# Optimization experiments

Hardware: AMD Instinct MI355X
Metric: run time of the kernel (lower is better)

Reference implementation:

```python
import jax, jax.numpy as jnp
import numpy as np

B, T, NC, NK, H, W = 2, 4, 3, 16, 180, 320
K = 3
PAD = 1
SCALE = 4
K2 = K * K
CIN_D = T * NK  # deformable conv input channels = group_of_frames * num_kernels


def conv2d(x, w, b=None, pad=PAD):
    y = jax.lax.conv_general_dilated(
        x, w, (1, 1), [(pad, pad), (pad, pad)],
        dimension_numbers=('NCHW', 'OIHW', 'NCHW'))
    if b is not None:
        y = y + b[None, :, None, None]
    return y


def convlstm(X, w, b, W_ci, W_cf, W_co):
    # X: (B, T, NC, H, W) -> (B, T, NK, H, W); peephole ConvLSTM
    Bn = X.shape[0]
    h0 = jnp.zeros((Bn, NK, H, W), X.dtype)
    c0 = jnp.zeros_like(h0)

    def step(carry, xt):
        h, c = carry
        g = conv2d(jnp.concatenate([xt, h], axis=1), w, b)  # (B, 4*NK, H, W)
        ig, fg, cg, og = jnp.split(g, 4, axis=1)
        i = jax.nn.sigmoid(ig + W_ci * c)
        f = jax.nn.sigmoid(fg + W_cf * c)
        c = f * c + i * jnp.tanh(cg)
        o = jax.nn.sigmoid(og + W_co * c)
        h = o * jnp.tanh(c)
        return (h, c), h

    _, hs = jax.lax.scan(step, (h0, c0), jnp.swapaxes(X, 0, 1))
    return jnp.swapaxes(hs, 0, 1)  # (B, T, NK, H, W)


def deform_conv(x, off_w, off_b, mod_w, mod_b, w, b):
    # Modulated deformable conv v2 (torchvision deform_conv2d semantics)
    Bn, Cin, Hi, Wi = x.shape
    off = conv2d(x, off_w, off_b).reshape(Bn, K2, 2, Hi, Wi)  # (dy, dx) per tap
    mask = 2.0 * jax.nn.sigmoid(conv2d(x, mod_w, mod_b))       # (B, K2, H, W)
    dy, dx = off[:, :, 0], off[:, :, 1]
    ky, kx = jnp.meshgrid(jnp.arange(K), jnp.arange(K), indexing='ij')
    base_y = jnp.arange(Hi, dtype=x.dtype)[None, None, :, None] - PAD + ky.reshape(1, K2, 1, 1).astype(x.dtype)
    base_x = jnp.arange(Wi, dtype=x.dtype)[None, None, None, :] - PAD + kx.reshape(1, K2, 1, 1).astype(x.dtype)
    py = base_y + dy  # (B, K2, H, W) float sampling positions
    px = base_x + dx
    y0 = jnp.floor(py)
    x0 = jnp.floor(px)

    def gather(yi, xi):
        valid = ((yi >= 0) & (yi < Hi) & (xi >= 0) & (xi < Wi)).astype(x.dtype)
        yc = jnp.clip(yi, 0, Hi - 1).astype(jnp.int32)
        xc = jnp.clip(xi, 0, Wi - 1).astype(jnp.int32)
        v = jax.vmap(lambda xb, yb, xib: xb[:, yb, xib])(x, yc, xc)  # (B, C, K2, H, W)
        return v * valid[:, None]

    wy1 = py - y0
    wx1 = px - x0
    samp = (((1 - wy1) * (1 - wx1))[:, None] * gather(y0, x0)
            + ((1 - wy1) * wx1)[:, None] * gather(y0, x0 + 1)
            + (wy1 * (1 - wx1))[:, None] * gather(y0 + 1, x0)
            + (wy1 * wx1)[:, None] * gather(y0 + 1, x0 + 1))
    samp = samp * mask[:, None]  # (B, Cin, K2, H, W)
    out = jnp.einsum('bckhw,ock->bohw', samp, w.reshape(w.shape[0], Cin, K2))
    return out + b[None, :, None, None]


def pixel_shuffle(x, r):
    Bn, Crr, Hi, Wi = x.shape
    C = Crr // (r * r)
    x = x.reshape(Bn, C, r, r, Hi, Wi).transpose(0, 1, 4, 2, 5, 3)
    return x.reshape(Bn, C, Hi * r, Wi * r)


def setup_inputs() -> dict:
    key = jax.random.key(0)
    ks = jax.random.split(key, 16)
    s = lambda k, shape, sc=0.05: jax.random.normal(k, shape, jnp.float32) * sc
    return {
        'X': jax.random.uniform(ks[0], (B, T, NC, H, W), jnp.float32),
        'lstm_w': s(ks[1], (4 * NK, NC + NK, K, K)),
        'lstm_b': s(ks[2], (4 * NK,)),
        'W_ci': s(ks[3], (NK, H, W)),
        'W_cf': s(ks[4], (NK, H, W)),
        'W_co': s(ks[5], (NK, H, W)),
        'off_w': s(ks[6], (2 * K2, CIN_D, K, K), 0.01),
        'off_b': jnp.zeros((2 * K2,), jnp.float32),
        'mod_w': s(ks[7], (K2, CIN_D, K, K), 0.01),
        'mod_b': jnp.zeros((K2,), jnp.float32),
        'def_w': s(ks[8], (NK, CIN_D, K, K)),
        'def_b': s(ks[9], (NK,)),
        'out_w': s(ks[10], (NC * SCALE ** 2, NK, K, K)),
        'out_b': s(ks[11], (NC * SCALE ** 2,)),
    }


def reference(X, lstm_w, lstm_b, W_ci, W_cf, W_co, off_w, off_b, mod_w, mod_b, def_w, def_b, out_w, out_b):
    hs = convlstm(X, lstm_w, lstm_b, W_ci, W_cf, W_co)   # (B, T, NK, H, W)
    x = hs.reshape(hs.shape[0], T * NK, H, W)            # chunk(dim=1)+squeeze+cat(dim=1)
    x = deform_conv(x, off_w, off_b, mod_w, mod_b, def_w, def_b)  # (B, NK, H, W)
    x = conv2d(x, out_w, out_b)                          # (B, NC*scale^2, H, W)
    return jnp.clip(pixel_shuffle(x, SCALE), 0.0, 255.0)
```

## Files before the change

### kernel.cpp

```cpp
#include <hip/hip_runtime.h>
#include <hip/hip_bf16.h>

#define Bn 2
#define Tn 4
#define NCc 3
#define NKc 16
#define Hc 180
#define Wc 320
#define HWc (Hc * Wc)
#define NPIX (Bn * HWc)
#define CIN_LSTM 19
#define GATES 64
#define CIN_D 64
#define TAPS_L (CIN_LSTM * 9)
#define TAPS_D (CIN_D * 9)
#define TAPS_O (NKc * 9)

typedef __hip_bfloat16 bf16;
typedef float f32x4 __attribute__((ext_vector_type(4)));
typedef float f32x2 __attribute__((ext_vector_type(2)));

__device__ __forceinline__ float getv(const float* p, long i) { return p[i]; }
__device__ __forceinline__ float getv(const bf16* p, long i) {
    unsigned int u = ((unsigned int)((const unsigned short*)p)[i]) << 16;
    return __uint_as_float(u);
}
__device__ __forceinline__ void putv(float* p, long i, float v) { p[i] = v; }
__device__ __forceinline__ void putv(bf16* p, long i, float v) { p[i] = __float2bfloat16(v); }
__device__ __forceinline__ float sigm(float x) { return 1.0f / (1.0f + __expf(-x)); }
__device__ __forceinline__ float tanh_(float x) { return 1.0f - 2.0f / (__expf(2.0f * x) + 1.0f); }

__device__ __forceinline__ void load4(const float* row, int x0, float* d) {
    const float4 v = *(const float4*)(row + x0);
    d[0] = v.x; d[1] = v.y; d[2] = v.z; d[3] = v.w;
}
__device__ __forceinline__ void load4(const bf16* row, int x0, float* d) {
    ushort4 u = *(const ushort4*)((const unsigned short*)row + x0);
    d[0] = __uint_as_float(((unsigned int)u.x) << 16);
    d[1] = __uint_as_float(((unsigned int)u.y) << 16);
    d[2] = __uint_as_float(((unsigned int)u.z) << 16);
    d[3] = __uint_as_float(((unsigned int)u.w) << 16);
}

__device__ __forceinline__ int xcd_chunked(int i, int nwg) {
    int q = nwg >> 3, r = nwg & 7;
    int xcd = i & 7, idx = i >> 3;
    return (xcd < r ? xcd * (q + 1) : r * (q + 1) + (xcd - r) * q) + idx;
}

__device__ __forceinline__ void om_wait()
{
    asm volatile("s_waitcnt vmcnt(0)" ::: "memory");
    __builtin_amdgcn_sched_barrier(0);
}

__device__ __forceinline__ void om_issue12(
    const float* p0, const float* p1, const float* p2,
    f32x4& a0, f32x4& b0, float& h00, float& h01,
    f32x4& a1, f32x4& b1, float& h10, float& h11,
    f32x4& a2, f32x4& b2, float& h20, float& h21)
{
    asm volatile(
        "global_load_dwordx4 %[A0], %[p0], off\n\t"
        "global_load_dwordx4 %[B0], %[p0], off offset:16\n\t"
        "global_load_dword   %[H00], %[p0], off offset:-4\n\t"
        "global_load_dword   %[H01], %[p0], off offset:32\n\t"
        "global_load_dwordx4 %[A1], %[p1], off\n\t"
        "global_load_dwordx4 %[B1], %[p1], off offset:16\n\t"
        "global_load_dword   %[H10], %[p1], off offset:-4\n\t"
        "global_load_dword   %[H11], %[p1], off offset:32\n\t"
        "global_load_dwordx4 %[A2], %[p2], off\n\t"
        "global_load_dwordx4 %[B2], %[p2], off offset:16\n\t"
        "global_load_dword   %[H20], %[p2], off offset:-4\n\t"
        "global_load_dword   %[H21], %[p2], off offset:32\n\t"
        : [A0]"=&v"(a0), [B0]"=&v"(b0), [H00]"=&v"(h00), [H01]"=&v"(h01),
          [A1]"=&v"(a1), [B1]"=&v"(b1), [H10]"=&v"(h10), [H11]"=&v"(h11),
          [A2]"=&v"(a2), [B2]"=&v"(b2), [H20]"=&v"(h20), [H21]"=&v"(h21)
        : [p0]"v"(p0), [p1]"v"(p1), [p2]"v"(p2));
}

__device__ __forceinline__ void lstm_issue12(
    const float* p0, const float* p1, const float* p2, const float* p3,
    f32x4& a0, float& l0, float& r0,
    f32x4& a1, float& l1, float& r1,
    f32x4& a2, float& l2, float& r2,
    f32x4& a3, float& l3, float& r3)
{
    asm volatile(
        "global_load_dwordx4 %[A0], %[P0], off\n\t"
        "global_load_dword   %[L0], %[P0], off offset:-4\n\t"
        "global_load_dword   %[R0], %[P0], off offset:16\n\t"
        "global_load_dwordx4 %[A1], %[P1], off\n\t"
        "global_load_dword   %[L1], %[P1], off offset:-4\n\t"
        "global_load_dword   %[R1], %[P1], off offset:16\n\t"
        "global_load_dwordx4 %[A2], %[P2], off\n\t"
        "global_load_dword   %[L2], %[P2], off offset:-4\n\t"
        "global_load_dword   %[R2], %[P2], off offset:16\n\t"
        "global_load_dwordx4 %[A3], %[P3], off\n\t"
        "global_load_dword   %[L3], %[P3], off offset:-4\n\t"
        "global_load_dword   %[R3], %[P3], off offset:16\n\t"
        : [A0]"=&v"(a0), [L0]"=&v"(l0), [R0]"=&v"(r0),
          [A1]"=&v"(a1), [L1]"=&v"(l1), [R1]"=&v"(r1),
          [A2]"=&v"(a2), [L2]"=&v"(l2), [R2]"=&v"(r2),
          [A3]"=&v"(a3), [L3]"=&v"(l3), [R3]"=&v"(r3)
        : [P0]"v"(p0), [P1]"v"(p1), [P2]"v"(p2), [P3]"v"(p3));
}

__device__ __forceinline__ void dfm_issue9w(
    const float* base, const int (&o)[9], f32x2 (&v)[9])
{
    asm volatile(
        "global_load_dwordx2 %[V0], %[O0], %[B]\n\t"
        "global_load_dwordx2 %[V1], %[O1], %[B]\n\t"
        "global_load_dwordx2 %[V2], %[O2], %[B]\n\t"
        "global_load_dwordx2 %[V3], %[O3], %[B]\n\t"
        "global_load_dwordx2 %[V4], %[O4], %[B]\n\t"
        "global_load_dwordx2 %[V5], %[O5], %[B]\n\t"
        "global_load_dwordx2 %[V6], %[O6], %[B]\n\t"
        "global_load_dwordx2 %[V7], %[O7], %[B]\n\t"
        "global_load_dwordx2 %[V8], %[O8], %[B]\n\t"
        : [V0]"=&v"(v[0]), [V1]"=&v"(v[1]), [V2]"=&v"(v[2]),
          [V3]"=&v"(v[3]), [V4]"=&v"(v[4]), [V5]"=&v"(v[5]),
          [V6]"=&v"(v[6]), [V7]"=&v"(v[7]), [V8]"=&v"(v[8])
        : [B]"s"(base),
          [O0]"v"(o[0]), [O1]"v"(o[1]), [O2]"v"(o[2]),
          [O3]"v"(o[3]), [O4]"v"(o[4]), [O5]"v"(o[5]),
          [O6]"v"(o[6]), [O7]"v"(o[7]), [O8]"v"(o[8]));
}

__global__ void __launch_bounds__(256) k_detect(const void* lstm_w_raw, int* flag)
{
    __shared__ int bad;
    if (threadIdx.x == 0) bad = 0;
    __syncthreads();
    const unsigned short* u = (const unsigned short*)lstm_w_raw;
    int local = 0;
    for (int i = threadIdx.x; i < GATES * TAPS_L; i += 256) {
        unsigned int f32 = ((unsigned int)u[i]) << 16;
        float v = __uint_as_float(f32);
        if (!(fabsf(v) <= 64.0f)) local = 1;
    }
    if (local) atomicOr(&bad, 1);
    __syncthreads();
    if (threadIdx.x == 0) flag[0] = bad ? 0 : 1;
}

template <typename S>
__device__ __forceinline__ void conv_plane2r(
    const S* __restrict__ src, int cin, int y0, int x0, int kc,
    const float* __restrict__ sw, float (&acc)[2][4][4])
{
    float xs[4][6];
#pragma unroll
    for (int r = 0; r < 4; r++) {
        int yy = y0 - 1 + r;
        if (yy >= 0 && yy < Hc) {
            const S* row = src + (long)yy * Wc;
            xs[r][0] = (x0 > 0) ? getv(row, x0 - 1) : 0.0f;
            load4(row, x0, &xs[r][1]);
            xs[r][5] = (x0 + 4 < Wc) ? getv(row, x0 + 4) : 0.0f;
        } else {
#pragma unroll
            for (int j = 0; j < 6; j++) xs[r][j] = 0.0f;
        }
    }
    float4 wq[9];
#pragma unroll
    for (int t9 = 0; t9 < 9; t9++)
        wq[t9] = *(const float4*)&sw[(((cin * 9 + t9) * 16) + kc) * 4];
#pragma unroll
    for (int ky = 0; ky < 3; ky++) {
#pragma unroll
        for (int kx = 0; kx < 3; kx++) {
            const float4 w = wq[ky * 3 + kx];
#pragma unroll
            for (int px = 0; px < 4; px++) {
                float v0 = xs[ky][px + kx];
                float v1 = xs[ky + 1][px + kx];
                acc[0][0][px] += w.x * v0;  acc[1][0][px] += w.x * v1;
                acc[0][1][px] += w.y * v0;  acc[1][1][px] += w.y * v1;
                acc[0][2][px] += w.z * v0;  acc[1][2][px] += w.z * v1;
                acc[0][3][px] += w.w * v0;  acc[1][3][px] += w.w * v1;
            }
        }
    }
}

template <typename T>
__device__ __forceinline__ void lstm2r_body(
    const T* __restrict__ X, const T* __restrict__ lstm_w, const T* __restrict__ lstm_b,
    const T* __restrict__ Wci, const T* __restrict__ Wcf, const T* __restrict__ Wco,
    float* __restrict__ c_buf, float* __restrict__ xcat, int t,
    float* sw, float* sb)
{
    for (int i = threadIdx.x; i < GATES * TAPS_L; i += 256) {
        int co = i / TAPS_L, tap = i - co * TAPS_L;
        int kc = co & 15, g = co >> 4;
        sw[(tap * 16 + kc) * 4 + g] = getv(lstm_w, i);
    }
    if (threadIdx.x < GATES) sb[threadIdx.x] = getv(lstm_b, threadIdx.x);
    __syncthreads();

    int blk = xcd_chunked(blockIdx.x, Bn * 90 * 5);
    int seg = blk % 5; int rem = blk / 5;
    int yp = rem % 90; int b = rem / 90;
    int y0 = yp * 2;
    int kc = threadIdx.x >> 4, pl = threadIdx.x & 15;
    int x0 = seg * 64 + pl * 4;

    float acc[2][4][4];
#pragma unroll
    for (int px = 0; px < 4; px++) {
#pragma unroll
        for (int r = 0; r < 2; r++) {
            acc[r][0][px] = sb[kc];
            acc[r][1][px] = sb[16 + kc];
            acc[r][2][px] = sb[32 + kc];
            acc[r][3][px] = sb[48 + kc];
        }
    }

    const T* xt = X + (long)(b * Tn + t) * NCc * HWc;
#pragma unroll 1
    for (int cin = 0; cin < NCc; cin++)
        conv_plane2r(xt + (long)cin * HWc, cin, y0, x0, kc, sw, acc);

    if (t > 0) {
        const float* hp = xcat + ((long)b * CIN_D + (t - 1) * NKc) * HWc;
        long ro[4]; float vm[4];
#pragma unroll
        for (int r = 0; r < 4; r++) {
            int yy = y0 - 1 + r;
            vm[r] = (yy >= 0 && yy < Hc) ? 1.0f : 0.0f;
            ro[r] = (long)min(max(yy, 0), Hc - 1) * Wc + x0;
        }
        const float m0 = (x0 > 0) ? 1.0f : 0.0f;
        const float m1 = (x0 + 4 < Wc) ? 1.0f : 0.0f;

#pragma unroll 1
        for (int cin = 0; cin < NKc; cin++) {
            const float* xc = hp + (long)cin * HWc;
            f32x4 a0, a1, a2, a3;
            float l0, l1, l2, l3, rh0, rh1, rh2, rh3;
            lstm_issue12(xc + ro[0], xc + ro[1], xc + ro[2], xc + ro[3],
                         a0, l0, rh0, a1, l1, rh1, a2, l2, rh2, a3, l3, rh3);
            float4 wq[9];
#pragma unroll
            for (int t9 = 0; t9 < 9; t9++)
                wq[t9] = *(const float4*)&sw[((((cin + NCc) * 9 + t9) * 16) + kc) * 4];
            om_wait();
            float xs[4][6];
#pragma unroll
            for (int r = 0; r < 4; r++) {
                const f32x4 a = (r == 0) ? a0 : (r == 1) ? a1 : (r == 2) ? a2 : a3;
                const float ll = (r == 0) ? l0 : (r == 1) ? l1 : (r == 2) ? l2 : l3;
                const float rr = (r == 0) ? rh0 : (r == 1) ? rh1 : (r == 2) ? rh2 : rh3;
                xs[r][0] = ll * vm[r] * m0;
                xs[r][1] = a.x * vm[r]; xs[r][2] = a.y * vm[r];
                xs[r][3] = a.z * vm[r]; xs[r][4] = a.w * vm[r];
                xs[r][5] = rr * vm[r] * m1;
            }
#pragma unroll
            for (int ky = 0; ky < 3; ky++) {
#pragma unroll
                for (int kx = 0; kx < 3; kx++) {
                    const float4 w = wq[ky * 3 + kx];
#pragma unroll
                    for (int px = 0; px < 4; px++) {
                        float v0 = xs[ky][px + kx];
                        float v1 = xs[ky + 1][px + kx];
                        acc[0][0][px] += w.x * v0;  acc[1][0][px] += w.x * v1;
                        acc[0][1][px] += w.y * v0;  acc[1][1][px] += w.y * v1;
                        acc[0][2][px] += w.z * v0;  acc[1][2][px] += w.z * v1;
                        acc[0][3][px] += w.w * v0;  acc[1][3][px] += w.w * v1;
                    }
                }
            }
        }
    }

#pragma unroll
    for (int r = 0; r < 2; r++) {
        int y = y0 + r;
        long pbase = (long)y * Wc + x0;
        float* cb = c_buf + (long)(b * NKc + kc) * HWc + pbase;
        float cprev[4];
        if (t > 0) {
            const float4 cv = *(const float4*)cb;
            cprev[0] = cv.x; cprev[1] = cv.y; cprev[2] = cv.z; cprev[3] = cv.w;
        } else {
            cprev[0] = cprev[1] = cprev[2] = cprev[3] = 0.0f;
        }
        float wci[4], wcf[4], wco[4];
        load4(Wci + (long)kc * HWc + pbase, 0, wci);
        load4(Wcf + (long)kc * HWc + pbase, 0, wcf);
        load4(Wco + (long)kc * HWc + pbase, 0, wco);

        float cn4[4], h4[4];
#pragma unroll
        for (int px = 0; px < 4; px++) {
            float ii = sigm(acc[r][0][px] + wci[px] * cprev[px]);
            float ff = sigm(acc[r][1][px] + wcf[px] * cprev[px]);
            float cn = ff * cprev[px] + ii * tanh_(acc[r][2][px]);
            float oo = sigm(acc[r][3][px] + wco[px] * cn);
            cn4[px] = cn; h4[px] = oo * tanh_(cn);
        }
        *(float4*)cb = make_float4(cn4[0], cn4[1], cn4[2], cn4[3]);
        *(float4*)(xcat + ((long)b * CIN_D + t * NKc + kc) * HWc + pbase) =
            make_float4(h4[0], h4[1], h4[2], h4[3]);
    }
}

__global__ void __launch_bounds__(256) k_lstm2(
    const void* X, const void* lstm_w, const void* lstm_b,
    const void* Wci, const void* Wcf, const void* Wco,
    const int* __restrict__ flag,
    float* c_buf, float* xcat, int t)
{
    __shared__ float sw[TAPS_L * GATES];
    __shared__ float sb[GATES];
    if (flag[0])
        lstm2r_body<bf16>((const bf16*)X, (const bf16*)lstm_w, (const bf16*)lstm_b,
                          (const bf16*)Wci, (const bf16*)Wcf, (const bf16*)Wco,
                          c_buf, xcat, t, sw, sb);
    else
        lstm2r_body<float>((const float*)X, (const float*)lstm_w, (const float*)lstm_b,
                           (const float*)Wci, (const float*)Wcf, (const float*)Wco,
                           c_buf, xcat, t, sw, sb);
}

template <typename T>
__device__ __forceinline__ void offmod12_body(
    const float* __restrict__ xcat,
    const T* __restrict__ off_w, const T* __restrict__ off_b,
    const T* __restrict__ mod_w, const T* __restrict__ mod_b,
    float* __restrict__ offbuf, float* __restrict__ maskbuf,
    float* sw, float* sb)
{
    int rb = xcd_chunked(blockIdx.x, 450);
    int type = rb & 1;
    int chunk = rb >> 1;
    const int nslot = type ? 12 : 16;

    for (int i = threadIdx.x; i < TAPS_D * nslot; i += 256) {
        int tap = i / nslot, j = i - tap * nslot;
        int o = type ? 16 + j : j;
        float v = 0.0f;
        if (o < 18) v = getv(off_w, (long)o * TAPS_D + tap);
        else if (o < 27) v = getv(mod_w, (long)(o - 18) * TAPS_D + tap);
        sw[tap * nslot + j] = v;
    }
    if (threadIdx.x < nslot) {
        int o = (type ? 16 : 0) + threadIdx.x;
        sb[threadIdx.x] = (o < 18) ? getv(off_b, o)
                        : (o < 27 ? getv(mod_b, o - 18) : 0.0f);
    }
    __syncthreads();

    int og = threadIdx.x >> 6, lane = threadIdx.x & 63;
    long p0 = (long)chunk * 512 + lane * 8;
    int b = (int)(p0 / HWc);
    int p = (int)(p0 - (long)b * HWc);
    int y = p / Wc, x0 = p - (p / Wc) * Wc;

    const int per = type ? 3 : 4;
    int jbase = og * per;

    const float* xb = xcat + (long)b * CIN_D * HWc;
    long yo[3]; float vm[3];
#pragma unroll
    for (int ky = 0; ky < 3; ky++) {
        int yy = y + ky - 1;
        vm[ky] = (yy >= 0 && yy < Hc) ? 1.0f : 0.0f;
        yo[ky] = (long)min(max(yy, 0), Hc - 1) * Wc + x0;
    }
    const float m0 = (x0 > 0) ? 1.0f : 0.0f;
    const float m1 = (x0 + 8 < Wc) ? 1.0f : 0.0f;

    float acc[4][8];
#pragma unroll
    for (int j = 0; j < 4; j++) {
        float bv = (j < per) ? sb[jbase + j] : 0.0f;
#pragma unroll
        for (int px = 0; px < 8; px++) acc[j][px] = bv;
    }

    if (type == 0) {
#pragma unroll 1
        for (int cin = 0; cin < CIN_D; cin++) {
            const float* xc = xb + (long)cin * HWc;
            f32x4 a0, b0v, a1, b1v, a2, b2v;
            float h00, h01, h10, h11, h20, h21;
            om_issue12(xc + yo[0], xc + yo[1], xc + yo[2],
                       a0, b0v, h00, h01, a1, b1v, h10, h11, a2, b2v, h20, h21);
            float4 wr[9];
#pragma unroll
            for (int t9 = 0; t9 < 9; t9++)
                wr[t9] = *(const float4*)&sw[(cin * 9 + t9) * 16 + jbase];
            om_wait();
            float xs[3][10];
#pragma unroll
            for (int ky = 0; ky < 3; ky++) {
                const f32x4 a = (ky == 0) ? a0 : (ky == 1) ? a1 : a2;
                const f32x4 bb = (ky == 0) ? b0v : (ky == 1) ? b1v : b2v;
                const float hh0 = (ky == 0) ? h00 : (ky == 1) ? h10 : h20;
                const float hh1 = (ky == 0) ? h01 : (ky == 1) ? h11 : h21;
                xs[ky][0] = hh0 * vm[ky] * m0;
                xs[ky][1] = a.x * vm[ky]; xs[ky][2] = a.y * vm[ky];
                xs[ky][3] = a.z * vm[ky]; xs[ky][4] = a.w * vm[ky];
                xs[ky][5] = bb.x * vm[ky]; xs[ky][6] = bb.y * vm[ky];
                xs[ky][7] = bb.z * vm[ky]; xs[ky][8] = bb.w * vm[ky];
                xs[ky][9] = hh1 * vm[ky] * m1;
            }
#pragma unroll
            for (int ky = 0; ky < 3; ky++) {
#pragma unroll
                for (int kx = 0; kx < 3; kx++) {
                    const float4 wq = wr[ky * 3 + kx];
#pragma unroll
                    for (int px = 0; px < 8; px++) {
                        float v = xs[ky][px + kx];
                        acc[0][px] += wq.x * v;
                        acc[1][px] += wq.y * v;
                        acc[2][px] += wq.z * v;
                        acc[3][px] += wq.w * v;
                    }
                }
            }
        }
    } else {
#pragma unroll 1
        for (int cin = 0; cin < CIN_D; cin++) {
            const float* xc = xb + (long)cin * HWc;
            f32x4 a0, b0v, a1, b1v, a2, b2v;
            float h00, h01, h10, h11, h20, h21;
            om_issue12(xc + yo[0], xc + yo[1], xc + yo[2],
                       a0, b0v, h00, h01, a1, b1v, h10, h11, a2, b2v, h20, h21);
            float3 wr[9];
#pragma unroll
            for (int t9 = 0; t9 < 9; t9++) {
                const float* wp = &sw[(cin * 9 + t9) * 12 + jbase];
                wr[t9] = make_float3(wp[0], wp[1], wp[2]);
            }
            om_wait();
            float xs[3][10];
#pragma unroll
            for (int ky = 0; ky < 3; ky++) {
                const f32x4 a = (ky == 0) ? a0 : (ky == 1) ? a1 : a2;
                const f32x4 bb = (ky == 0) ? b0v : (ky == 1) ? b1v : b2v;
                const float hh0 = (ky == 0) ? h00 : (ky == 1) ? h10 : h20;
                const float hh1 = (ky == 0) ? h01 : (ky == 1) ? h11 : h21;
                xs[ky][0] = hh0 * vm[ky] * m0;
                xs[ky][1] = a.x * vm[ky]; xs[ky][2] = a.y * vm[ky];
                xs[ky][3] = a.z * vm[ky]; xs[ky][4] = a.w * vm[ky];
                xs[ky][5] = bb.x * vm[ky]; xs[ky][6] = bb.y * vm[ky];
                xs[ky][7] = bb.z * vm[ky]; xs[ky][8] = bb.w * vm[ky];
                xs[ky][9] = hh1 * vm[ky] * m1;
            }
#pragma unroll
            for (int ky = 0; ky < 3; ky++) {
#pragma unroll
                for (int kx = 0; kx < 3; kx++) {
                    const float3 wq = wr[ky * 3 + kx];
#pragma unroll
                    for (int px = 0; px < 8; px++) {
                        float v = xs[ky][px + kx];
                        acc[0][px] += wq.x * v;
                        acc[1][px] += wq.y * v;
                        acc[2][px] += wq.z * v;
                    }
                }
            }
        }
    }

    long pbase = (long)y * Wc + x0;
#pragma unroll
    for (int j = 0; j < 4; j++) {
        if (j >= per) break;
        int o = (type ? 16 : 0) + jbase + j;
        if (o >= 27) break;
        if (o < 18) {
            float* dst = offbuf + ((long)b * 18 + o) * HWc + pbase;
            *(float4*)dst = make_float4(acc[j][0], acc[j][1], acc[j][2], acc[j][3]);
            *(float4*)(dst + 4) = make_float4(acc[j][4], acc[j][5], acc[j][6], acc[j][7]);
        } else {
            float* dst = maskbuf + ((long)b * 9 + (o - 18)) * HWc + pbase;
            *(float4*)dst = make_float4(2.0f * sigm(acc[j][0]), 2.0f * sigm(acc[j][1]),
                                        2.0f * sigm(acc[j][2]), 2.0f * sigm(acc[j][3]));
            *(float4*)(dst + 4) = make_float4(2.0f * sigm(acc[j][4]), 2.0f * sigm(acc[j][5]),
                                              2.0f * sigm(acc[j][6]), 2.0f * sigm(acc[j][7]));
        }
    }
}

__global__ void __launch_bounds__(256) k_offmod(
    const float* xcat, const void* off_w, const void* off_b,
    const void* mod_w, const void* mod_b, const int* __restrict__ flag,
    float* offbuf, float* maskbuf)
{
    __shared__ float sw[TAPS_D * 16];
    __shared__ float sb[16];
    if (flag[0])
        offmod12_body<bf16>(xcat, (const bf16*)off_w, (const bf16*)off_b,
                            (const bf16*)mod_w, (const bf16*)mod_b, offbuf, maskbuf, sw, sb);
    else
        offmod12_body<float>(xcat, (const float*)off_w, (const float*)off_b,
                             (const float*)mod_w, (const float*)mod_b, offbuf, maskbuf, sw, sb);
}

template <typename T>
__device__ __forceinline__ void deform5_body(
    const float* __restrict__ xcat, const float* __restrict__ offbuf,
    const float* __restrict__ maskbuf,
    const T* __restrict__ def_w, const T* __restrict__ def_b,
    float* __restrict__ dcout, float* sw, float* sb)
{
    for (int i = threadIdx.x; i < NKc * TAPS_D; i += 256) {
        int co = i / TAPS_D;
        int tap = i - co * TAPS_D;
        sw[tap * NKc + co] = getv(def_w, i);
    }
    if (threadIdx.x < NKc) sb[threadIdx.x] = getv(def_b, threadIdx.x);
    __syncthreads();

    int blk = xcd_chunked(blockIdx.x, NPIX / 256);
    int idx0 = blk * 256;
    int b = idx0 / HWc;
    int p = idx0 - b * HWc + threadIdx.x;
    int y = p / Wc, x = p - (p / Wc) * Wc;

    float w00[9], w01[9], w10[9], w11[9];
    int o0[9], o1[9];
    float sel[9];
#pragma unroll
    for (int k = 0; k < 9; k++) {
        int ky = k / 3, kx = k - (k / 3) * 3;
        float dy = offbuf[((long)b * 18 + 2 * k) * HWc + p];
        float dx = offbuf[((long)b * 18 + 2 * k + 1) * HWc + p];
        float m = maskbuf[((long)b * 9 + k) * HWc + p];
        float py = (float)(y - 1 + ky) + dy;
        float px = (float)(x - 1 + kx) + dx;
        float y0f = floorf(py), x0f = floorf(px);
        int y0 = (int)y0f, x0 = (int)x0f;
        float wy1 = py - y0f, wx1 = px - x0f;
        float a00 = (1.0f - wy1) * (1.0f - wx1) * m;
        float a01 = (1.0f - wy1) * wx1 * m;
        float a10 = wy1 * (1.0f - wx1) * m;
        float a11 = wy1 * wx1 * m;
        bool vy0 = (y0 >= 0) && (y0 < Hc);
        bool vy1 = (y0 + 1 >= 0) && (y0 + 1 < Hc);
        bool vx0 = (x0 >= 0) && (x0 < Wc);
        bool vx1 = (x0 + 1 >= 0) && (x0 + 1 < Wc);
        w00[k] = (vy0 && vx0) ? a00 : 0.0f;
        w01[k] = (vy0 && vx1) ? a01 : 0.0f;
        w10[k] = (vy1 && vx0) ? a10 : 0.0f;
        w11[k] = (vy1 && vx1) ? a11 : 0.0f;
        int yc0 = min(max(y0, 0), Hc - 1);
        int yc1 = min(max(y0 + 1, 0), Hc - 1);
        int xc0 = min(max(x0, 0), Wc - 1);
        int xc1 = min(max(x0 + 1, 0), Wc - 1);
        o0[k] = (yc0 * Wc + xc0) * 4;
        o1[k] = (yc1 * Wc + xc0) * 4;
        sel[k] = (xc1 > xc0) ? 1.0f : 0.0f;
    }

    float acc[NKc];
#pragma unroll
    for (int i = 0; i < NKc; i++) acc[i] = sb[i];

    const float* xb = xcat + (long)b * CIN_D * HWc;
#pragma unroll 1
    for (int cin = 0; cin < CIN_D; cin++) {
        const float* xc = xb + (long)cin * HWc;
        f32x2 u0[9], u1[9];
        dfm_issue9w(xc, o0, u0);
        dfm_issue9w(xc, o1, u1);
        om_wait();
        float s[9];
#pragma unroll
        for (int k = 0; k < 9; k++) {
            float v01 = u0[k].x + sel[k] * (u0[k].y - u0[k].x);
            float v11 = u1[k].x + sel[k] * (u1[k].y - u1[k].x);
            s[k] = w00[k] * u0[k].x + w01[k] * v01 +
                   w10[k] * u1[k].x + w11[k] * v11;
        }
#pragma unroll
        for (int k = 0; k < 9; k++) {
            const float* wrow = &sw[(cin * 9 + k) * NKc];
#pragma unroll
            for (int co = 0; co < NKc; co++) acc[co] += wrow[co] * s[k];
        }
    }

#pragma unroll
    for (int co = 0; co < NKc; co++)
        dcout[((long)b * NKc + co) * HWc + p] = acc[co];
}

__global__ void __launch_bounds__(256) k_deform(
    const float* xcat, const float* offbuf, const float* maskbuf,
    const void* def_w, const void* def_b, const int* __restrict__ flag,
    float* dcout)
{
    __shared__ float sw[TAPS_D * NKc];
    __shared__ float sb[NKc];
    if (flag[0])
        deform5_body<bf16>(xcat, offbuf, maskbuf, (const bf16*)def_w, (const bf16*)def_b,
                           dcout, sw, sb);
    else
        deform5_body<float>(xcat, offbuf, maskbuf, (const float*)def_w, (const float*)def_b,
                            dcout, sw, sb);
}

template <typename T>
__device__ __forceinline__ void outconv6_body(
    const float* __restrict__ dcout, const T* __restrict__ out_w,
    const T* __restrict__ out_b, T* __restrict__ out, float* sw, float* sb)
{
    int rb = xcd_chunked(blockIdx.x, 900);
    int type = rb & 1;
    int chunk = rb >> 1;

    for (int i = threadIdx.x; i < 24 * TAPS_O; i += 256) {
        int o = i / TAPS_O, tap = i - o * TAPS_O;
        int slot = (o / 6) * 8 + (o % 6);
        sw[tap * 32 + slot] = getv(out_w, (long)(type * 24 + o) * TAPS_O + tap);
    }
    if (threadIdx.x < 24) sb[threadIdx.x] = getv(out_b, type * 24 + threadIdx.x);
    __syncthreads();

    int og = threadIdx.x >> 6, lane = threadIdx.x & 63;
    long p0 = ((long)chunk * 64 + lane) * 4;
    int b = (int)(p0 / HWc);
    int p = (int)(p0 - (long)b * HWc);
    int y = p / Wc, x0 = p - (p / Wc) * Wc;

    float acc[6][4];
#pragma unroll
    for (int j = 0; j < 6; j++) {
        float bv = sb[og * 6 + j];
#pragma unroll
        for (int px = 0; px < 4; px++) acc[j][px] = bv;
    }

    const float* xb = dcout + (long)b * NKc * HWc;
#pragma unroll 1
    for (int cin = 0; cin < NKc; cin++) {
        const float* xc = xb + (long)cin * HWc;
        float xs[3][6];
#pragma unroll
        for (int ky = 0; ky < 3; ky++) {
            int yy = y + ky - 1;
            if (yy >= 0 && yy < Hc) {
                const float* row = xc + (long)yy * Wc;
                xs[ky][0] = (x0 > 0) ? row[x0 - 1] : 0.0f;
                load4(row, x0, &xs[ky][1]);
                xs[ky][5] = (x0 + 4 < Wc) ? row[x0 + 4] : 0.0f;
            } else {
#pragma unroll
                for (int j = 0; j < 6; j++) xs[ky][j] = 0.0f;
            }
        }
        float4 wa[9]; float2 wb[9];
#pragma unroll
        for (int t9 = 0; t9 < 9; t9++) {
            const float* wp = &sw[(cin * 9 + t9) * 32 + og * 8];
            wa[t9] = *(const float4*)wp;
            wb[t9] = *(const float2*)(wp + 4);
        }
#pragma unroll
        for (int ky = 0; ky < 3; ky++) {
#pragma unroll
            for (int kx = 0; kx < 3; kx++) {
                const float4 w0 = wa[ky * 3 + kx];
                const float2 w1 = wb[ky * 3 + kx];
#pragma unroll
                for (int px = 0; px < 4; px++) {
                    float v = xs[ky][px + kx];
                    acc[0][px] += w0.x * v;  acc[1][px] += w0.y * v;
                    acc[2][px] += w0.z * v;  acc[3][px] += w0.w * v;
                    acc[4][px] += w1.x * v;  acc[5][px] += w1.y * v;
                }
            }
        }
    }

#pragma unroll
    for (int j = 0; j < 6; j++) {
        int co = type * 24 + og * 6 + j;
        int cc = co >> 4;
        int r = co & 15;
        int ii = r >> 2, jj = r & 3;
        long ob = (((long)b * 3 + cc) * (Hc * 4) + (y * 4 + ii)) * (long)(Wc * 4);
#pragma unroll
        for (int px = 0; px < 4; px++) {
            float v = fminf(fmaxf(acc[j][px], 0.0f), 255.0f);
            putv(out, ob + (x0 + px) * 4 + jj, v);
        }
    }
}

__global__ void __launch_bounds__(256) k_outconv(
    const float* dcout, const void* out_w, const void* out_b,
    const int* __restrict__ flag, void* out)
{
    __shared__ float sw[TAPS_O * 32];
    __shared__ float sb[24];
    if (flag[0])
        outconv6_body<bf16>(dcout, (const bf16*)out_w, (const bf16*)out_b, (bf16*)out, sw, sb);
    else
        outconv6_body<float>(dcout, (const float*)out_w, (const float*)out_b, (float*)out, sw, sb);
}

extern "C" void kernel_launch(void* const* d_in, const int* in_sizes, int n_in,
                              void* d_out, int out_size, void* d_ws, size_t ws_size,
                              hipStream_t stream) {
    const void* X      = d_in[0];
    const void* lstm_w = d_in[1];
    const void* lstm_b = d_in[2];
    const void* Wci    = d_in[3];
    const void* Wcf    = d_in[4];
    const void* Wco    = d_in[5];
    const void* off_w  = d_in[6];
    const void* off_b  = d_in[7];
    const void* mod_w  = d_in[8];
    const void* mod_b  = d_in[9];
    const void* def_w  = d_in[10];
    const void* def_b  = d_in[11];
    const void* out_w  = d_in[12];
    const void* out_b  = d_in[13];

    int* flag = (int*)d_ws;
    float* W = (float*)d_ws + 64;
    size_t o = 0;
    float* c_buf   = W + o; o += (size_t)Bn * NKc * HWc;
    float* xcat    = W + o; o += (size_t)Bn * CIN_D * HWc;
    float* offbuf  = W + o; o += (size_t)Bn * 18 * HWc;
    float* maskbuf = W + o; o += (size_t)Bn * 9 * HWc;
    float* dcout   = W + o; o += (size_t)Bn * NKc * HWc;

    dim3 blk(256);
    dim3 gridP(NPIX / 256);
    dim3 gridL2(Bn * (Hc / 2) * 5);
    dim3 gridOM(2 * (NPIX / 512));
    dim3 gridC2(2 * (NPIX / 4 / 64));

    k_detect<<<1, blk, 0, stream>>>(lstm_w, flag);
    for (int t = 0; t < Tn; t++) {
        k_lstm2<<<gridL2, blk, 0, stream>>>(X, lstm_w, lstm_b, Wci, Wcf, Wco,
                                            flag, c_buf, xcat, t);
    }
    k_offmod<<<gridOM, blk, 0, stream>>>(xcat, off_w, off_b, mod_w, mod_b, flag,
                                         offbuf, maskbuf);
    k_deform<<<gridP, blk, 0, stream>>>(xcat, offbuf, maskbuf, def_w, def_b, flag, dcout);
    k_outconv<<<gridC2, blk, 0, stream>>>(dcout, out_w, out_b, flag, d_out);
}
```

Baseline: 592.1 us.

## Use coalesced 4-pixel lane groups with shuffle-based halos in offset/mask conv

Each lane in the offset/mask conv now loads two 4-pixel groups that are 256 pixels apart, instead of 8 contiguous pixels. A wave's dwordx4 loads therefore cover contiguous 1 KB spans. Left and right halo values come from neighbouring lanes through cross-lane shuffles, and only the block's edge pixels get separate scalar loads. The aim is better load coalescing and fewer redundant halo loads, at the cost of added shuffle instructions and more setup. The type-0 and type-1 loops are also merged into one loop with a branch inside it.

```diff
diff --git a/kernel.cpp b/kernel.cpp
--- a/kernel.cpp
+++ b/kernel.cpp
@@ -54,29 +54,35 @@
     __builtin_amdgcn_sched_barrier(0);
 }
 
-__device__ __forceinline__ void om_issue12(
-    const float* p0, const float* p1, const float* p2,
-    f32x4& a0, f32x4& b0, float& h00, float& h01,
-    f32x4& a1, f32x4& b1, float& h10, float& h11,
-    f32x4& a2, f32x4& b2, float& h20, float& h21)
+__device__ __forceinline__ void om13_issue(
+    const float* a0p, const float* a1p, const float* a2p,
+    const float* b0p, const float* b1p, const float* b2p,
+    const float* l0p, const float* l1p, const float* l2p,
+    const float* r0p, const float* r1p, const float* r2p,
+    f32x4& A0, f32x4& A1, f32x4& A2, f32x4& B0, f32x4& B1, f32x4& B2,
+    float& l0, float& l1, float& l2, float& r0, float& r1, float& r2)
 {
     asm volatile(
-        "global_load_dwordx4 %[A0], %[p0], off\n\t"
-        "global_load_dwordx4 %[B0], %[p0], off offset:16\n\t"
-        "global_load_dword   %[H00], %[p0], off offset:-4\n\t"
-        "global_load_dword   %[H01], %[p0], off offset:32\n\t"
-        "global_load_dwordx4 %[A1], %[p1], off\n\t"
-        "global_load_dwordx4 %[B1], %[p1], off offset:16\n\t"
-        "global_load_dword   %[H10], %[p1], off offset:-4\n\t"
-        "global_load_dword   %[H11], %[p1], off offset:32\n\t"
-        "global_load_dwordx4 %[A2], %[p2], off\n\t"
-        "global_load_dwordx4 %[B2], %[p2], off offset:16\n\t"
-        "global_load_dword   %[H20], %[p2], off offset:-4\n\t"
-        "global_load_dword   %[H21], %[p2], off offset:32\n\t"
-        : [A0]"=&v"(a0), [B0]"=&v"(b0), [H00]"=&v"(h00), [H01]"=&v"(h01),
-          [A1]"=&v"(a1), [B1]"=&v"(b1), [H10]"=&v"(h10), [H11]"=&v"(h11),
-          [A2]"=&v"(a2), [B2]"=&v"(b2), [H20]"=&v"(h20), [H21]"=&v"(h21)
-        : [p0]"v"(p0), [p1]"v"(p1), [p2]"v"(p2));
+        "global_load_dwordx4 %[A0], %[a0], off\n\t"
+        "global_load_dwordx4 %[A1], %[a1], off\n\t"
+        "global_load_dwordx4 %[A2], %[a2], off\n\t"
+        "global_load_dwordx4 %[B0], %[b0], off\n\t"
+        "global_load_dwordx4 %[B1], %[b1], off\n\t"
+        "global_load_dwordx4 %[B2], %[b2], off\n\t"
+        "global_load_dword %[L0], %[l0p], off\n\t"
+        "global_load_dword %[L1], %[l1p], off\n\t"
+        "global_load_dword %[L2], %[l2p], off\n\t"
+        "global_load_dword %[R0], %[r0p], off\n\t"
+        "global_load_dword %[R1], %[r1p], off\n\t"
+        "global_load_dword %[R2], %[r2p], off\n\t"
+        : [A0]"=&v"(A0), [A1]"=&v"(A1), [A2]"=&v"(A2),
+          [B0]"=&v"(B0), [B1]"=&v"(B1), [B2]"=&v"(B2),
+          [L0]"=&v"(l0), [L1]"=&v"(l1), [L2]"=&v"(l2),
+          [R0]"=&v"(r0), [R1]"=&v"(r1), [R2]"=&v"(r2)
+        : [a0]"v"(a0p), [a1]"v"(a1p), [a2]"v"(a2p),
+          [b0]"v"(b0p), [b1]"v"(b1p), [b2]"v"(b2p),
+          [l0p]"v"(l0p), [l1p]"v"(l1p), [l2p]"v"(l2p),
+          [r0p]"v"(r0p), [r1p]"v"(r1p), [r2p]"v"(r2p));
 }
 
 __device__ __forceinline__ void lstm_issue12(
@@ -330,7 +336,7 @@
 }
 
 template <typename T>
-__device__ __forceinline__ void offmod12_body(
+__device__ __forceinline__ void offmod13_body(
     const float* __restrict__ xcat,
     const T* __restrict__ off_w, const T* __restrict__ off_b,
     const T* __restrict__ mod_w, const T* __restrict__ mod_b,
@@ -358,138 +364,173 @@
     __syncthreads();
 
     int og = threadIdx.x >> 6, lane = threadIdx.x & 63;
-    long p0 = (long)chunk * 512 + lane * 8;
-    int b = (int)(p0 / HWc);
-    int p = (int)(p0 - (long)b * HWc);
-    int y = p / Wc, x0 = p - (p / Wc) * Wc;
+
+    long pg[2]; pg[0] = (long)chunk * 512 + 4 * lane; pg[1] = pg[0] + 256;
+    int bg[2], ppg[2];
+    int yo[2][3]; float vm[2][3], mL[2], mR[2];
+    const float* xbg[2];
+#pragma unroll
+    for (int g = 0; g < 2; g++) {
+        int b = (int)(pg[g] / HWc);
+        int pp = (int)(pg[g] - (long)b * HWc);
+        int y = pp / Wc, x = pp - (pp / Wc) * Wc;
+        bg[g] = b; ppg[g] = pp;
+        xbg[g] = xcat + (long)b * CIN_D * HWc;
+#pragma unroll
+        for (int ky = 0; ky < 3; ky++) {
+            int yy = y + ky - 1;
+            vm[g][ky] = (yy >= 0 && yy < Hc) ? 1.0f : 0.0f;
+            yo[g][ky] = min(max(yy, 0), Hc - 1) * Wc + x;
+        }
+        mL[g] = (x > 0) ? 1.0f : 0.0f;
+        mR[g] = (x + 4 < Wc) ? 1.0f : 0.0f;
+    }
+    const float *eLp[3], *eRp[3];
+    {
+        long pL = (long)chunk * 512;
+        int b = (int)(pL / HWc); int pp = (int)(pL - (long)b * HWc);
+        int y = pp / Wc, x = pp - (pp / Wc) * Wc;
+#pragma unroll
+        for (int ky = 0; ky < 3; ky++)
+            eLp[ky] = xcat + (long)b * CIN_D * HWc
+                    + (long)min(max(y + ky - 1, 0), Hc - 1) * Wc + x - 1;
+        long pR = (long)chunk * 512 + 511;
+        b = (int)(pR / HWc); pp = (int)(pR - (long)b * HWc);
+        y = pp / Wc; x = pp - (pp / Wc) * Wc;
+#pragma unroll
+        for (int ky = 0; ky < 3; ky++)
+            eRp[ky] = xcat + (long)b * CIN_D * HWc
+                    + (long)min(max(y + ky - 1, 0), Hc - 1) * Wc + x + 1;
+    }
 
     const int per = type ? 3 : 4;
     int jbase = og * per;
-
-    const float* xb = xcat + (long)b * CIN_D * HWc;
-    long yo[3]; float vm[3];
-#pragma unroll
-    for (int ky = 0; ky < 3; ky++) {
-        int yy = y + ky - 1;
-        vm[ky] = (yy >= 0 && yy < Hc) ? 1.0f : 0.0f;
-        yo[ky] = (long)min(max(yy, 0), Hc - 1) * Wc + x0;
-    }
-    const float m0 = (x0 > 0) ? 1.0f : 0.0f;
-    const float m1 = (x0 + 8 < Wc) ? 1.0f : 0.0f;
-
-    float acc[4][8];
+    const int upl = (lane + 63) & 63, dnl = (lane + 1) & 63;
+
+    float acc[4][2][4];
 #pragma unroll
     for (int j = 0; j < 4; j++) {
         float bv = (j < per) ? sb[jbase + j] : 0.0f;
 #pragma unroll
-        for (int px = 0; px < 8; px++) acc[j][px] = bv;
-    }
-
-    if (type == 0) {
+        for (int g = 0; g < 2; g++)
+#pragma unroll
+            for (int px = 0; px < 4; px++) acc[j][g][px] = bv;
+    }
+
 #pragma unroll 1
-        for (int cin = 0; cin < CIN_D; cin++) {
-            const float* xc = xb + (long)cin * HWc;
-            f32x4 a0, b0v, a1, b1v, a2, b2v;
-            float h00, h01, h10, h11, h20, h21;
-            om_issue12(xc + yo[0], xc + yo[1], xc + yo[2],
-                       a0, b0v, h00, h01, a1, b1v, h10, h11, a2, b2v, h20, h21);
-            float4 wr[9];
+    for (int cin = 0; cin < CIN_D; cin++) {
+        const long coff = (long)cin * HWc;
+        const float* c0 = xbg[0] + coff;
+        const float* c1 = xbg[1] + coff;
+        f32x4 A[3], B[3]; float el[3], er[3];
+        om13_issue(c0 + yo[0][0], c0 + yo[0][1], c0 + yo[0][2],
+                   c1 + yo[1][0], c1 + yo[1][1], c1 + yo[1][2],
+                   eLp[0] + coff, eLp[1] + coff, eLp[2] + coff,
+                   eRp[0] + coff, eRp[1] + coff, eRp[2] + coff,
+                   A[0], A[1], A[2], B[0], B[1], B[2],
+                   el[0], el[1], el[2], er[0], er[1], er[2]);
+        float4 wr4[9]; float3 wr3[9];
+        if (type == 0) {
 #pragma unroll
             for (int t9 = 0; t9 < 9; t9++)
-                wr[t9] = *(const float4*)&sw[(cin * 9 + t9) * 16 + jbase];
-            om_wait();
-            float xs[3][10];
+                wr4[t9] = *(const float4*)&sw[(cin * 9 + t9) * 16 + jbase];
+        } else {
+#pragma unroll
+            for (int t9 = 0; t9 < 9; t9++) {
+                const float* wp = &sw[(cin * 9 + t9) * 12 + jbase];
+                wr3[t9] = make_float3(wp[0], wp[1], wp[2]);
+            }
+        }
+        om_wait();
+
+        float xs0[3][6], xs1[3][6];
+#pragma unroll
+        for (int ky = 0; ky < 3; ky++) {
+            float aw = A[ky].w, ax = A[ky].x, bw = B[ky].w, bx = B[ky].x;
+            float sAw = __shfl(aw, upl);
+            float sAx = __shfl(ax, dnl);
+            float sBw = __shfl(bw, upl);
+            float sBx = __shfl(bx, dnl);
+            float B0x = __shfl(bx, 0);
+            float A63w = __shfl(aw, 63);
+            float g0l = (lane == 0) ? el[ky] : sAw;
+            float g0r = (lane == 63) ? B0x : sAx;
+            float g1l = (lane == 0) ? A63w : sBw;
+            float g1r = (lane == 63) ? er[ky] : sBx;
+            float v0 = vm[0][ky], v1 = vm[1][ky];
+            xs0[ky][0] = g0l * v0 * mL[0];
+            xs0[ky][1] = A[ky].x * v0; xs0[ky][2] = A[ky].y * v0;
+            xs0[ky][3] = A[ky].z * v0; xs0[ky][4] = A[ky].w * v0;
+            xs0[ky][5] = g0r * v0 * mR[0];
+            xs1[ky][0] = g1l * v1 * mL[1];
+            xs1[ky][1] = B[ky].x * v1; xs1[ky][2] = B[ky].y * v1;
+            xs1[ky][3] = B[ky].z * v1; xs1[ky][4] = B[ky].w * v1;
+            xs1[ky][5] = g1r * v1 * mR[1];
+        }
+
+        if (type == 0) {
 #pragma unroll
             for (int ky = 0; ky < 3; ky++) {
-                const f32x4 a = (ky == 0) ? a0 : (ky == 1) ? a1 : a2;
-                const f32x4 bb = (ky == 0) ? b0v : (ky == 1) ? b1v : b2v;
-                const float hh0 = (ky == 0) ? h00 : (ky == 1) ? h10 : h20;
-                const float hh1 = (ky == 0) ? h01 : (ky == 1) ? h11 : h21;
-                xs[ky][0] = hh0 * vm[ky] * m0;
-                xs[ky][1] = a.x * vm[ky]; xs[ky][2] = a.y * vm[ky];
-                xs[ky][3] = a.z * vm[ky]; xs[ky][4] = a.w * vm[ky];
-                xs[ky][5] = bb.x * vm[ky]; xs[ky][6] = bb.y * vm[ky];
-                xs[ky][7] = bb.z * vm[ky]; xs[ky][8] = bb.w * vm[ky];
-                xs[ky][9] = hh1 * vm[ky] * m1;
-            }
-#pragma unroll
-            for (int ky = 0; ky < 3; ky++) {
 #pragma unroll
                 for (int kx = 0; kx < 3; kx++) {
-                    const float4 wq = wr[ky * 3 + kx];
-#pragma unroll
-                    for (int px = 0; px < 8; px++) {
-                        float v = xs[ky][px + kx];
-                        acc[0][px] += wq.x * v;
-                        acc[1][px] += wq.y * v;
-                        acc[2][px] += wq.z * v;
-                        acc[3][px] += wq.w * v;
+                    const float4 wq = wr4[ky * 3 + kx];
+#pragma unroll
+                    for (int px = 0; px < 4; px++) {
+                        float u = xs0[ky][px + kx];
+                        acc[0][0][px] += wq.x * u;
+                        acc[1][0][px] += wq.y * u;
+                        acc[2][0][px] += wq.z * u;
+                        acc[3][0][px] += wq.w * u;
+                        float w2 = xs1[ky][px + kx];
+                        acc[0][1][px] += wq.x * w2;
+                        acc[1][1][px] += wq.y * w2;
+                        acc[2][1][px] += wq.z * w2;
+                        acc[3][1][px] += wq.w * w2;
                     }
                 }
             }
-        }
-    } else {
-#pragma unroll 1
-        for (int cin = 0; cin < CIN_D; cin++) {
-            const float* xc = xb + (long)cin * HWc;
-            f32x4 a0, b0v, a1, b1v, a2, b2v;
-            float h00, h01, h10, h11, h20, h21;
-            om_issue12(xc + yo[0], xc + yo[1], xc + yo[2],
-                       a0, b0v, h00, h01, a1, b1v, h10, h11, a2, b2v, h20, h21);
-            float3 wr[9];
-#pragma unroll
-            for (int t9 = 0; t9 < 9; t9++) {
-                const float* wp = &sw[(cin * 9 + t9) * 12 + jbase];
-                wr[t9] = make_float3(wp[0], wp[1], wp[2]);
-            }
-            om_wait();
-            float xs[3][10];
+        } else {
 #pragma unroll
             for (int ky = 0; ky < 3; ky++) {
-                const f32x4 a = (ky == 0) ? a0 : (ky == 1) ? a1 : a2;
-                const f32x4 bb = (ky == 0) ? b0v : (ky == 1) ? b1v : b2v;
-                const float hh0 = (ky == 0) ? h00 : (ky == 1) ? h10 : h20;
-                const float hh1 = (ky == 0) ? h01 : (ky == 1) ? h11 : h21;
-                xs[ky][0] = hh0 * vm[ky] * m0;
-                xs[ky][1] = a.x * vm[ky]; xs[ky][2] = a.y * vm[ky];
-                xs[ky][3] = a.z * vm[ky]; xs[ky][4] = a.w * vm[ky];
-                xs[ky][5] = bb.x * vm[ky]; xs[ky][6] = bb.y * vm[ky];
-                xs[ky][7] = bb.z * vm[ky]; xs[ky][8] = bb.w * vm[ky];
-                xs[ky][9] = hh1 * vm[ky] * m1;
-            }
-#pragma unroll
-            for (int ky = 0; ky < 3; ky++) {
 #pragma unroll
                 for (int kx = 0; kx < 3; kx++) {
-                    const float3 wq = wr[ky * 3 + kx];
-#pragma unroll
-                    for (int px = 0; px < 8; px++) {
-                        float v = xs[ky][px + kx];
-                        acc[0][px] += wq.x * v;
-                        acc[1][px] += wq.y * v;
-                        acc[2][px] += wq.z * v;
+                    const float3 wq = wr3[ky * 3 + kx];
+#pragma unroll
+                    for (int px = 0; px < 4; px++) {
+                        float u = xs0[ky][px + kx];
+                        acc[0][0][px] += wq.x * u;
+                        acc[1][0][px] += wq.y * u;
+                        acc[2][0][px] += wq.z * u;
+                        float w2 = xs1[ky][px + kx];
+                        acc[0][1][px] += wq.x * w2;
+                        acc[1][1][px] += wq.y * w2;
+                        acc[2][1][px] += wq.z * w2;
                     }
                 }
             }
         }
     }
 
-    long pbase = (long)y * Wc + x0;
 #pragma unroll
     for (int j = 0; j < 4; j++) {
         if (j >= per) break;
         int o = (type ? 16 : 0) + jbase + j;
         if (o >= 27) break;
         if (o < 18) {
-            float* dst = offbuf + ((long)b * 18 + o) * HWc + pbase;
-            *(float4*)dst = make_float4(acc[j][0], acc[j][1], acc[j][2], acc[j][3]);
-            *(float4*)(dst + 4) = make_float4(acc[j][4], acc[j][5], acc[j][6], acc[j][7]);
+#pragma unroll
+            for (int g = 0; g < 2; g++) {
+                float* dst = offbuf + ((long)bg[g] * 18 + o) * HWc + ppg[g];
+                *(float4*)dst = make_float4(acc[j][g][0], acc[j][g][1],
+                                            acc[j][g][2], acc[j][g][3]);
+            }
         } else {
-            float* dst = maskbuf + ((long)b * 9 + (o - 18)) * HWc + pbase;
-            *(float4*)dst = make_float4(2.0f * sigm(acc[j][0]), 2.0f * sigm(acc[j][1]),
-                                        2.0f * sigm(acc[j][2]), 2.0f * sigm(acc[j][3]));
-            *(float4*)(dst + 4) = make_float4(2.0f * sigm(acc[j][4]), 2.0f * sigm(acc[j][5]),
-                                              2.0f * sigm(acc[j][6]), 2.0f * sigm(acc[j][7]));
+#pragma unroll
+            for (int g = 0; g < 2; g++) {
+                float* dst = maskbuf + ((long)bg[g] * 9 + (o - 18)) * HWc + ppg[g];
+                *(float4*)dst = make_float4(
+                    2.0f * sigm(acc[j][g][0]), 2.0f * sigm(acc[j][g][1]),
+                    2.0f * sigm(acc[j][g][2]), 2.0f * sigm(acc[j][g][3]));
+            }
         }
     }
 }
@@ -502,10 +543,10 @@
     __shared__ float sw[TAPS_D * 16];
     __shared__ float sb[16];
     if (flag[0])
-        offmod12_body<bf16>(xcat, (const bf16*)off_w, (const bf16*)off_b,
+        offmod13_body<bf16>(xcat, (const bf16*)off_w, (const bf16*)off_b,
                             (const bf16*)mod_w, (const bf16*)mod_b, offbuf, maskbuf, sw, sb);
     else
-        offmod12_body<float>(xcat, (const float*)off_w, (const float*)off_b,
+        offmod13_body<float>(xcat, (const float*)off_w, (const float*)off_b,
                              (const float*)mod_w, (const float*)mod_b, offbuf, maskbuf, sw, sb);
 }
 
```

After: 575.6 us. 2.8% less time.
